# Kernel tuning notes

Measured on AMD Instinct MI355X. Metric: run time of the kernel, lower is better.

## Reference

```python
import jax, jax.numpy as jnp
import numpy as np

B, T, D = 2048, 240, 90  # batch, seq_len (hard-coded 240 in module), hidden
NCLS = 40


def setup_inputs() -> dict:
    key = jax.random.key(0)
    ks = jax.random.split(key, 7)
    s = 1.0 / np.sqrt(D)          # torch LSTMCell init bound
    so = 1.0 / np.sqrt(T * D)     # torch Linear init bound
    x = jax.random.normal(ks[0], (B, T, D), dtype=jnp.float32)
    W_ih = jax.random.uniform(ks[1], (4 * D, D), minval=-s, maxval=s, dtype=jnp.float32)
    W_hh = jax.random.uniform(ks[2], (4 * D, D), minval=-s, maxval=s, dtype=jnp.float32)
    b_ih = jax.random.uniform(ks[3], (4 * D,), minval=-s, maxval=s, dtype=jnp.float32)
    b_hh = jax.random.uniform(ks[4], (4 * D,), minval=-s, maxval=s, dtype=jnp.float32)
    W_out = jax.random.uniform(ks[5], (NCLS, T * D), minval=-so, maxval=so, dtype=jnp.float32)
    b_out = jax.random.uniform(ks[6], (NCLS,), minval=-so, maxval=so, dtype=jnp.float32)
    return {"x": x, "W_ih": W_ih, "W_hh": W_hh, "b_ih": b_ih, "b_hh": b_hh,
            "W_out": W_out, "b_out": b_out}


def reference(x, W_ih, W_hh, b_ih, b_hh, W_out, b_out):
    # The torch loop calls LSTMCell(x[:, i]) with DEFAULT zero (h0, c0) every
    # step -> no recurrence. W_hh @ h0 == 0 and f * c0 == 0, so:
    #   gates = x_t @ W_ih^T + b_ih + b_hh ; gate order i, f, g, o
    gates = jnp.einsum('btd,gd->btg', x, W_ih) + b_ih + b_hh  # [B, T, 4D]
    i_g, _f_g, g_g, o_g = jnp.split(gates, 4, axis=-1)
    c = jax.nn.sigmoid(i_g) * jnp.tanh(g_g)                   # i * g (f*c0 = 0)
    h = jax.nn.sigmoid(o_g) * jnp.tanh(c)                     # [B, T, D]
    out = h.reshape(-1, T * D) @ W_out.T + b_out              # [B, 40]
    out = out.reshape(-1, 4, 10)
    return jax.nn.softmax(out, axis=2)
```

## Files before the change

### kernel.cpp

```cpp
#include <hip/hip_runtime.h>
#include <hip/hip_bf16.h>

#define BB   2048
#define TT   240
#define DD   90
#define MM   (BB*TT)
#define KDIM (TT*DD)
#define NCLS 40
#define NPAD 48
#define KS2  45
#define KST  15

typedef __bf16 bf16x8 __attribute__((ext_vector_type(8)));
typedef float  f32x4  __attribute__((ext_vector_type(4)));

#define LOG2E  1.44269504f
#define LOG2E2 2.88539008f

__device__ __forceinline__ bf16x8 cvt8(float4 a, float4 b){
    bf16x8 r;
    r[0]=(__bf16)a.x; r[1]=(__bf16)a.y; r[2]=(__bf16)a.z; r[3]=(__bf16)a.w;
    r[4]=(__bf16)b.x; r[5]=(__bf16)b.y; r[6]=(__bf16)b.z; r[7]=(__bf16)b.w;
    return r;
}

__device__ __forceinline__ unsigned pack_bf16(float a, float b){
    unsigned u0 = (unsigned)__builtin_bit_cast(unsigned short, (__bf16)a);
    unsigned u1 = (unsigned)__builtin_bit_cast(unsigned short, (__bf16)b);
    return u0 | (u1 << 16);
}

__device__ __forceinline__ float sig_tanh(float a, float b){
    float ea = exp2f(-LOG2E*a);
    float Eb = exp2f(LOG2E2*b);
    return (Eb - 1.f) * __builtin_amdgcn_rcpf((1.f + ea)*(Eb + 1.f));
}

__global__ void pack1(const float* __restrict__ Wih,
                      const float* __restrict__ bih,
                      const float* __restrict__ bhh,
                      __bf16* __restrict__ wtb)
{
    int id = blockIdx.x*256 + threadIdx.x;
    if (id >= 288*13) return;
    int c  = id / 13;
    int k8 = id - c*13;
    int g  = c / 96, dd = c - g*96;
    int row = (g==0 ? dd : (g==1 ? 180+dd : 270+dd));
    float bv = 0.f, bhi = 0.f, blo = 0.f;
    if (dd < 90){
        bv  = bih[row] + bhh[row];
        bhi = (float)(__bf16)bv;
        blo = bv - bhi;
    }
    bf16x8 v;
    #pragma unroll
    for (int e = 0; e < 8; ++e){
        int k = k8*8 + e;
        float f = 0.f;
        if (dd < 90){
            if (k < 90)       f = Wih[row*90 + k];
            else if (k == 90) f = bhi;
            else if (k == 91) f = blo;
        }
        v[e] = (__bf16)f;
    }
    *(bf16x8*)(wtb + c*104 + k8*8) = v;
}

__global__ void pack2(const float* __restrict__ W2,
                      __bf16* __restrict__ w2hi,
                      __bf16* __restrict__ w2lo)
{
    int id = blockIdx.x*256 + threadIdx.x;
    if (id >= NPAD*2700) return;
    int n  = id / 2700;
    int k8 = id - n*2700;
    bf16x8 vh, vl;
    if (n < NCLS){
        #pragma unroll
        for (int e = 0; e < 8; ++e){
            float f = W2[(size_t)n*KDIM + k8*8 + e];
            __bf16 hb = (__bf16)f;
            vh[e] = hb;
            vl[e] = (__bf16)(f - (float)hb);
        }
    } else {
        #pragma unroll
        for (int e = 0; e < 8; ++e){ vh[e] = (__bf16)0.f; vl[e] = (__bf16)0.f; }
    }
    *(bf16x8*)(w2hi + (size_t)n*KDIM + k8*8) = vh;
    *(bf16x8*)(w2lo + (size_t)n*KDIM + k8*8) = vl;
}

__global__ __launch_bounds__(512, 2)
void k1_gates(const float* __restrict__ x,
              const __bf16* __restrict__ wtb,
              __bf16* __restrict__ h)
{
    __shared__ __align__(16) __bf16 wt[288*104];

    const int tid  = threadIdx.x;
    const int lane = tid & 63;
    const int wv   = tid >> 6;
    const int rg   = wv >> 1;
    const int nh   = wv & 1;
    const int l15  = lane & 15;
    const int kg   = lane >> 4;

    {
        const float4* src = (const float4*)wtb;
        float4* dst = (float4*)wt;
        #pragma unroll
        for (int i = 0; i < 8; ++i){
            int idx = tid + i*512;
            if (idx < 3744) dst[idx] = src[idx];
        }
    }
    __syncthreads();

    const int tbase = blockIdx.x * 15;

    float4 xr[6];
    float2 xe;
    {
        const float* p = x + ((size_t)tbase*64 + rg*16 + l15)*90;
        #pragma unroll
        for (int ks = 0; ks < 2; ++ks){
            xr[ks*2+0] = *(const float4*)(p + ks*32 + kg*8);
            xr[ks*2+1] = *(const float4*)(p + ks*32 + kg*8 + 4);
        }
        if (kg < 3){
            xr[4] = *(const float4*)(p + 64 + kg*8);
            xr[5] = *(const float4*)(p + 64 + kg*8 + 4);
        } else {
            xe = *(const float2*)(p + 88);
        }
    }

    for (int t = 0; t < 15; ++t){
        bf16x8 af[3];
        af[0] = cvt8(xr[0], xr[1]);
        af[1] = cvt8(xr[2], xr[3]);
        if (kg < 3){
            af[2] = cvt8(xr[4], xr[5]);
        } else {
            bf16x8 z;
            #pragma unroll
            for (int e = 0; e < 8; ++e) z[e] = (__bf16)0.f;
            z[0] = (__bf16)xe.x; z[1] = (__bf16)xe.y;
            z[2] = (__bf16)1.0f; z[3] = (__bf16)1.0f;
            af[2] = z;
        }

        f32x4 acc[3][3];
        #pragma unroll
        for (int g = 0; g < 3; ++g)
            #pragma unroll
            for (int j = 0; j < 3; ++j) acc[g][j] = f32x4{0.f,0.f,0.f,0.f};

        const __bf16* wbase = wt + (nh*48 + l15)*104 + 8*kg;
        #pragma unroll
        for (int g = 0; g < 3; ++g){
            #pragma unroll
            for (int j = 0; j < 3; ++j){
                const __bf16* wrow = wbase + (g*96 + j*16)*104;
                #pragma unroll
                for (int ks = 0; ks < 3; ++ks){
                    bf16x8 wv8 = *(const bf16x8*)(wrow + ks*32);
                    acc[g][j] = __builtin_amdgcn_mfma_f32_16x16x32_bf16(wv8, af[ks], acc[g][j], 0,0,0);
                }
            }
        }

        if (t < 14){
            const float* p = x + ((size_t)(tbase+t+1)*64 + rg*16 + l15)*90;
            #pragma unroll
            for (int ks = 0; ks < 2; ++ks){
                xr[ks*2+0] = *(const float4*)(p + ks*32 + kg*8);
                xr[ks*2+1] = *(const float4*)(p + ks*32 + kg*8 + 4);
            }
            if (kg < 3){
                xr[4] = *(const float4*)(p + 64 + kg*8);
                xr[5] = *(const float4*)(p + 64 + kg*8 + 4);
            } else {
                xe = *(const float2*)(p + 88);
            }
        }

        const size_t mrow = (size_t)(tbase+t)*64 + rg*16 + l15;
        __bf16* hp = h + mrow*90;
        #pragma unroll
        for (int j = 0; j < 3; ++j){
            int dd0 = nh*48 + j*16 + kg*4;
            float hv[4];
            #pragma unroll
            for (int r = 0; r < 4; ++r){
                float cc = sig_tanh(acc[0][j][r], acc[1][j][r]);
                hv[r]    = sig_tanh(acc[2][j][r], cc);
            }
            if (dd0 < 90)
                *(unsigned*)(hp + dd0) = pack_bf16(hv[0], hv[1]);
            if (dd0 + 2 < 90)
                *(unsigned*)(hp + dd0 + 2) = pack_bf16(hv[2], hv[3]);
        }
    }
}

__global__ __launch_bounds__(256)
void k2_out(const __bf16* __restrict__ h,
            const __bf16* __restrict__ w2hi,
            const __bf16* __restrict__ w2lo,
            float* __restrict__ part2)
{
    const int tid  = threadIdx.x;
    const int lane = tid & 63;
    const int wv   = tid >> 6;
    const int l15  = lane & 15;
    const int kg   = lane >> 4;
    const int m0   = (blockIdx.x*4 + wv) * 32;
    const int chunk= blockIdx.y;
    const size_t kbase = (size_t)chunk*(KST*32) + 8*kg;

    const __bf16* ha = h    + (size_t)(m0 + l15)*KDIM + kbase;
    const __bf16* hb = ha   + (size_t)16*KDIM;
    const __bf16* h0 = w2hi + (size_t)l15*KDIM + kbase;
    const __bf16* h1 = h0   + (size_t)16*KDIM;
    const __bf16* h2 = h0   + (size_t)32*KDIM;
    const __bf16* l0 = w2lo + (size_t)l15*KDIM + kbase;
    const __bf16* l1 = l0   + (size_t)16*KDIM;
    const __bf16* l2 = l0   + (size_t)32*KDIM;

    f32x4 acc00 = {0.f,0.f,0.f,0.f}, acc01 = acc00, acc02 = acc00;
    f32x4 acc10 = acc00, acc11 = acc00, acc12 = acc00;

    #pragma unroll
    for (int s = 0; s < KST; ++s){
        bf16x8 a0  = *(const bf16x8*)(ha + s*32);
        bf16x8 a1  = *(const bf16x8*)(hb + s*32);
        bf16x8 bh0 = *(const bf16x8*)(h0 + s*32);
        bf16x8 bh1 = *(const bf16x8*)(h1 + s*32);
        bf16x8 bh2 = *(const bf16x8*)(h2 + s*32);
        bf16x8 bl0 = *(const bf16x8*)(l0 + s*32);
        bf16x8 bl1 = *(const bf16x8*)(l1 + s*32);
        bf16x8 bl2 = *(const bf16x8*)(l2 + s*32);
        acc00 = __builtin_amdgcn_mfma_f32_16x16x32_bf16(a0, bh0, acc00, 0,0,0);
        acc01 = __builtin_amdgcn_mfma_f32_16x16x32_bf16(a0, bh1, acc01, 0,0,0);
        acc02 = __builtin_amdgcn_mfma_f32_16x16x32_bf16(a0, bh2, acc02, 0,0,0);
        acc10 = __builtin_amdgcn_mfma_f32_16x16x32_bf16(a1, bh0, acc10, 0,0,0);
        acc11 = __builtin_amdgcn_mfma_f32_16x16x32_bf16(a1, bh1, acc11, 0,0,0);
        acc12 = __builtin_amdgcn_mfma_f32_16x16x32_bf16(a1, bh2, acc12, 0,0,0);
        acc00 = __builtin_amdgcn_mfma_f32_16x16x32_bf16(a0, bl0, acc00, 0,0,0);
        acc01 = __builtin_amdgcn_mfma_f32_16x16x32_bf16(a0, bl1, acc01, 0,0,0);
        acc02 = __builtin_amdgcn_mfma_f32_16x16x32_bf16(a0, bl2, acc02, 0,0,0);
        acc10 = __builtin_amdgcn_mfma_f32_16x16x32_bf16(a1, bl0, acc10, 0,0,0);
        acc11 = __builtin_amdgcn_mfma_f32_16x16x32_bf16(a1, bl1, acc11, 0,0,0);
        acc12 = __builtin_amdgcn_mfma_f32_16x16x32_bf16(a1, bl2, acc12, 0,0,0);
    }

    float* pp = part2 + (size_t)chunk*(BB*NPAD);
    const int rbase = kg*4;
    #pragma unroll
    for (int r = 0; r < 4; ++r){
        size_t row0 = (size_t)(m0 + rbase + r)*NPAD;
        size_t row1 = (size_t)(m0 + 16 + rbase + r)*NPAD;
        pp[row0 +      l15] = acc00[r];
        pp[row0 + 16 + l15] = acc01[r];
        pp[row0 + 32 + l15] = acc02[r];
        pp[row1 +      l15] = acc10[r];
        pp[row1 + 16 + l15] = acc11[r];
        pp[row1 + 32 + l15] = acc12[r];
    }
}

__global__ void k3a(const float* __restrict__ part2,
                    const float* __restrict__ bout,
                    float* __restrict__ logits)
{
    int g = blockIdx.x*256 + threadIdx.x;
    float s = 0.f;
    for (int c = 0; c < KS2; ++c) s += part2[(size_t)c*(BB*NPAD) + g];
    int n = g % NPAD;
    logits[g] = s + (n < NCLS ? bout[n] : 0.f);
}

__global__ void k3b(const float* __restrict__ logits, float* __restrict__ out)
{
    int b = blockIdx.x*256 + threadIdx.x;
    if (b >= BB) return;
    const float* lg = logits + (size_t)b*NPAD;
    #pragma unroll
    for (int g = 0; g < 4; ++g){
        float v[10]; float mx = -1e30f;
        #pragma unroll
        for (int q = 0; q < 10; ++q){ v[q] = lg[g*10+q]; mx = fmaxf(mx, v[q]); }
        float e[10]; float s = 0.f;
        #pragma unroll
        for (int q = 0; q < 10; ++q){ e[q] = __expf(v[q]-mx); s += e[q]; }
        float inv = 1.0f/s;
        #pragma unroll
        for (int q = 0; q < 10; ++q) out[(size_t)b*NCLS + g*10 + q] = e[q]*inv;
    }
}

extern "C" void kernel_launch(void* const* d_in, const int* in_sizes, int n_in,
                              void* d_out, int out_size, void* d_ws, size_t ws_size,
                              hipStream_t stream)
{
    const float* x    = (const float*)d_in[0];
    const float* Wih  = (const float*)d_in[1];
    const float* bih  = (const float*)d_in[3];
    const float* bhh  = (const float*)d_in[4];
    const float* W2   = (const float*)d_in[5];
    const float* bout = (const float*)d_in[6];
    float* out = (float*)d_out;

    char* ws = (char*)d_ws;
    size_t off = 0;
    auto alloc = [&](size_t bytes){ void* p = ws + off; off = (off + bytes + 255) & ~(size_t)255; return p; };
    __bf16* h     = (__bf16*)alloc((size_t)MM*DD*2);
    float*  part2 = (float*) alloc((size_t)KS2*BB*NPAD*4);
    float*  logits= (float*) alloc((size_t)BB*NPAD*4);
    __bf16* wtb   = (__bf16*)alloc(288*104*2);
    __bf16* w2hi  = (__bf16*)alloc((size_t)NPAD*KDIM*2);
    __bf16* w2lo  = (__bf16*)alloc((size_t)NPAD*KDIM*2);

    pack1<<<15, 256, 0, stream>>>(Wih, bih, bhh, wtb);
    pack2<<<(NPAD*2700 + 255)/256, 256, 0, stream>>>(W2, w2hi, w2lo);
    k1_gates<<<512, 512, 0, stream>>>(x, wtb, h);
    k2_out<<<dim3(16, KS2), 256, 0, stream>>>(h, w2hi, w2lo, part2);
    k3a<<<(BB*NPAD)/256, 256, 0, stream>>>(part2, bout, logits);
    k3b<<<(BB + 255)/256, 256, 0, stream>>>(logits, out);
}
```

Measured before the change: 138.4 us.

## Pad hidden rows to 96, reorder x prefetch before MFMA, fuse reduction and softmax

The h intermediate is stored with a row stride of 96 instead of 90, so k1 writes full aligned 8-byte chunks without bounds checks, and W_out is repacked with zero-padded columns to match. k2 now covers 16 k-steps per chunk over the padded K. The next x load is issued before the MFMA block so global latency overlaps compute. The split-K reduction and the softmax are fused into one kernel using shared memory, which drops the logits buffer and one launch. The cost is about 7% more bytes for h and for the W_out copies, plus extra MFMA work on the padded zeros.

```diff
diff --git a/kernel.cpp b/kernel.cpp
--- a/kernel.cpp
+++ b/kernel.cpp
@@ -4,12 +4,14 @@
 #define BB   2048
 #define TT   240
 #define DD   90
+#define HD   96
 #define MM   (BB*TT)
 #define KDIM (TT*DD)
+#define KD2  (TT*HD)
 #define NCLS 40
 #define NPAD 48
 #define KS2  45
-#define KST  15
+#define KST  16
 
 typedef __bf16 bf16x8 __attribute__((ext_vector_type(8)));
 typedef float  f32x4  __attribute__((ext_vector_type(4)));
@@ -73,24 +75,22 @@
                       __bf16* __restrict__ w2lo)
 {
     int id = blockIdx.x*256 + threadIdx.x;
-    if (id >= NPAD*2700) return;
-    int n  = id / 2700;
-    int k8 = id - n*2700;
+    if (id >= NPAD*(KD2/8)) return;
+    int n  = id / (KD2/8);
+    int k8 = id - n*(KD2/8);
+    int t  = k8 / 12;
+    int d0 = (k8 - t*12) * 8;
     bf16x8 vh, vl;
-    if (n < NCLS){
-        #pragma unroll
-        for (int e = 0; e < 8; ++e){
-            float f = W2[(size_t)n*KDIM + k8*8 + e];
-            __bf16 hb = (__bf16)f;
-            vh[e] = hb;
-            vl[e] = (__bf16)(f - (float)hb);
-        }
-    } else {
-        #pragma unroll
-        for (int e = 0; e < 8; ++e){ vh[e] = (__bf16)0.f; vl[e] = (__bf16)0.f; }
-    }
-    *(bf16x8*)(w2hi + (size_t)n*KDIM + k8*8) = vh;
-    *(bf16x8*)(w2lo + (size_t)n*KDIM + k8*8) = vl;
+    #pragma unroll
+    for (int e = 0; e < 8; ++e){
+        int d = d0 + e;
+        float f = (n < NCLS && d < 90) ? W2[(size_t)n*KDIM + t*90 + d] : 0.f;
+        __bf16 hb = (__bf16)f;
+        vh[e] = hb;
+        vl[e] = (__bf16)(f - (float)hb);
+    }
+    *(bf16x8*)(w2hi + (size_t)n*KD2 + k8*8) = vh;
+    *(bf16x8*)(w2lo + (size_t)n*KD2 + k8*8) = vl;
 }
 
 __global__ __launch_bounds__(512, 2)
@@ -151,26 +151,6 @@
             z[0] = (__bf16)xe.x; z[1] = (__bf16)xe.y;
             z[2] = (__bf16)1.0f; z[3] = (__bf16)1.0f;
             af[2] = z;
-        }
-
-        f32x4 acc[3][3];
-        #pragma unroll
-        for (int g = 0; g < 3; ++g)
-            #pragma unroll
-            for (int j = 0; j < 3; ++j) acc[g][j] = f32x4{0.f,0.f,0.f,0.f};
-
-        const __bf16* wbase = wt + (nh*48 + l15)*104 + 8*kg;
-        #pragma unroll
-        for (int g = 0; g < 3; ++g){
-            #pragma unroll
-            for (int j = 0; j < 3; ++j){
-                const __bf16* wrow = wbase + (g*96 + j*16)*104;
-                #pragma unroll
-                for (int ks = 0; ks < 3; ++ks){
-                    bf16x8 wv8 = *(const bf16x8*)(wrow + ks*32);
-                    acc[g][j] = __builtin_amdgcn_mfma_f32_16x16x32_bf16(wv8, af[ks], acc[g][j], 0,0,0);
-                }
-            }
         }
 
         if (t < 14){
@@ -188,8 +168,28 @@
             }
         }
 
+        f32x4 acc[3][3];
+        #pragma unroll
+        for (int g = 0; g < 3; ++g)
+            #pragma unroll
+            for (int j = 0; j < 3; ++j) acc[g][j] = f32x4{0.f,0.f,0.f,0.f};
+
+        const __bf16* wbase = wt + (nh*48 + l15)*104 + 8*kg;
+        #pragma unroll
+        for (int g = 0; g < 3; ++g){
+            #pragma unroll
+            for (int j = 0; j < 3; ++j){
+                const __bf16* wrow = wbase + (g*96 + j*16)*104;
+                #pragma unroll
+                for (int ks = 0; ks < 3; ++ks){
+                    bf16x8 wv8 = *(const bf16x8*)(wrow + ks*32);
+                    acc[g][j] = __builtin_amdgcn_mfma_f32_16x16x32_bf16(wv8, af[ks], acc[g][j], 0,0,0);
+                }
+            }
+        }
+
         const size_t mrow = (size_t)(tbase+t)*64 + rg*16 + l15;
-        __bf16* hp = h + mrow*90;
+        __bf16* hp = h + mrow*HD;
         #pragma unroll
         for (int j = 0; j < 3; ++j){
             int dd0 = nh*48 + j*16 + kg*4;
@@ -199,10 +199,10 @@
                 float cc = sig_tanh(acc[0][j][r], acc[1][j][r]);
                 hv[r]    = sig_tanh(acc[2][j][r], cc);
             }
-            if (dd0 < 90)
-                *(unsigned*)(hp + dd0) = pack_bf16(hv[0], hv[1]);
-            if (dd0 + 2 < 90)
-                *(unsigned*)(hp + dd0 + 2) = pack_bf16(hv[2], hv[3]);
+            uint2 pk;
+            pk.x = pack_bf16(hv[0], hv[1]);
+            pk.y = pack_bf16(hv[2], hv[3]);
+            *(uint2*)(hp + dd0) = pk;
         }
     }
 }
@@ -222,14 +222,14 @@
     const int chunk= blockIdx.y;
     const size_t kbase = (size_t)chunk*(KST*32) + 8*kg;
 
-    const __bf16* ha = h    + (size_t)(m0 + l15)*KDIM + kbase;
-    const __bf16* hb = ha   + (size_t)16*KDIM;
-    const __bf16* h0 = w2hi + (size_t)l15*KDIM + kbase;
-    const __bf16* h1 = h0   + (size_t)16*KDIM;
-    const __bf16* h2 = h0   + (size_t)32*KDIM;
-    const __bf16* l0 = w2lo + (size_t)l15*KDIM + kbase;
-    const __bf16* l1 = l0   + (size_t)16*KDIM;
-    const __bf16* l2 = l0   + (size_t)32*KDIM;
+    const __bf16* ha = h    + (size_t)(m0 + l15)*KD2 + kbase;
+    const __bf16* hb = ha   + (size_t)16*KD2;
+    const __bf16* h0 = w2hi + (size_t)l15*KD2 + kbase;
+    const __bf16* h1 = h0   + (size_t)16*KD2;
+    const __bf16* h2 = h0   + (size_t)32*KD2;
+    const __bf16* l0 = w2lo + (size_t)l15*KD2 + kbase;
+    const __bf16* l1 = l0   + (size_t)16*KD2;
+    const __bf16* l2 = l0   + (size_t)32*KD2;
 
     f32x4 acc00 = {0.f,0.f,0.f,0.f}, acc01 = acc00, acc02 = acc00;
     f32x4 acc10 = acc00, acc11 = acc00, acc12 = acc00;
@@ -273,33 +273,38 @@
     }
 }
 
-__global__ void k3a(const float* __restrict__ part2,
-                    const float* __restrict__ bout,
-                    float* __restrict__ logits)
-{
-    int g = blockIdx.x*256 + threadIdx.x;
-    float s = 0.f;
-    for (int c = 0; c < KS2; ++c) s += part2[(size_t)c*(BB*NPAD) + g];
-    int n = g % NPAD;
-    logits[g] = s + (n < NCLS ? bout[n] : 0.f);
-}
-
-__global__ void k3b(const float* __restrict__ logits, float* __restrict__ out)
-{
-    int b = blockIdx.x*256 + threadIdx.x;
-    if (b >= BB) return;
-    const float* lg = logits + (size_t)b*NPAD;
-    #pragma unroll
-    for (int g = 0; g < 4; ++g){
+__global__ __launch_bounds__(384)
+void k3(const float* __restrict__ part2,
+        const float* __restrict__ bout,
+        float* __restrict__ out)
+{
+    __shared__ float sm[8*NPAD];
+    const int tid  = threadIdx.x;
+    const int base = blockIdx.x * 8 * NPAD;
+
+    {
+        int g = base + tid;
+        float s = 0.f;
+        for (int c = 0; c < KS2; ++c) s += part2[(size_t)c*(BB*NPAD) + g];
+        int n = tid % NPAD;
+        sm[tid] = s + (n < NCLS ? bout[n] : 0.f);
+    }
+    __syncthreads();
+
+    if (tid < 32){
+        int lb  = tid >> 2;
+        int grp = tid & 3;
+        const float* lg = sm + lb*NPAD + grp*10;
         float v[10]; float mx = -1e30f;
         #pragma unroll
-        for (int q = 0; q < 10; ++q){ v[q] = lg[g*10+q]; mx = fmaxf(mx, v[q]); }
+        for (int q = 0; q < 10; ++q){ v[q] = lg[q]; mx = fmaxf(mx, v[q]); }
         float e[10]; float s = 0.f;
         #pragma unroll
         for (int q = 0; q < 10; ++q){ e[q] = __expf(v[q]-mx); s += e[q]; }
         float inv = 1.0f/s;
-        #pragma unroll
-        for (int q = 0; q < 10; ++q) out[(size_t)b*NCLS + g*10 + q] = e[q]*inv;
+        size_t b = (size_t)blockIdx.x*8 + lb;
+        #pragma unroll
+        for (int q = 0; q < 10; ++q) out[b*NCLS + grp*10 + q] = e[q]*inv;
     }
 }
 
@@ -318,17 +323,15 @@
     char* ws = (char*)d_ws;
     size_t off = 0;
     auto alloc = [&](size_t bytes){ void* p = ws + off; off = (off + bytes + 255) & ~(size_t)255; return p; };
-    __bf16* h     = (__bf16*)alloc((size_t)MM*DD*2);
+    __bf16* h     = (__bf16*)alloc((size_t)MM*HD*2);
     float*  part2 = (float*) alloc((size_t)KS2*BB*NPAD*4);
-    float*  logits= (float*) alloc((size_t)BB*NPAD*4);
     __bf16* wtb   = (__bf16*)alloc(288*104*2);
-    __bf16* w2hi  = (__bf16*)alloc((size_t)NPAD*KDIM*2);
-    __bf16* w2lo  = (__bf16*)alloc((size_t)NPAD*KDIM*2);
+    __bf16* w2hi  = (__bf16*)alloc((size_t)NPAD*KD2*2);
+    __bf16* w2lo  = (__bf16*)alloc((size_t)NPAD*KD2*2);
 
     pack1<<<15, 256, 0, stream>>>(Wih, bih, bhh, wtb);
-    pack2<<<(NPAD*2700 + 255)/256, 256, 0, stream>>>(W2, w2hi, w2lo);
+    pack2<<<(NPAD*(KD2/8) + 255)/256, 256, 0, stream>>>(W2, w2hi, w2lo);
     k1_gates<<<512, 512, 0, stream>>>(x, wtb, h);
     k2_out<<<dim3(16, KS2), 256, 0, stream>>>(h, w2hi, w2lo, part2);
-    k3a<<<(BB*NPAD)/256, 256, 0, stream>>>(part2, bout, logits);
-    k3b<<<(BB + 255)/256, 256, 0, stream>>>(logits, out);
-}
+    k3<<<BB/8, 384, 0, stream>>>(part2, bout, out);
+}
```

Result: slower. 146.4 us (+5.8%).

## Shrink gate-weight LDS stride, fold exp scales into weights, fuse reduce+softmax

Applied to the files above, without the earlier changes.

The packed W_ih tile in shared memory goes from a 104-element row stride to a dense 92-element stride, which shrinks LDS per block so more k1_gates blocks can share a CU (launch bounds raised to 6). The sigmoid/tanh exp2 scale factors are folded into the packed weights and bias, which removes multiplies from the activation epilogue. The split-K reduction and the softmax are fused into one kernel that stages logits in shared memory, dropping a launch and the logits round trip through global memory. Risks: the 92-element stride is not a multiple of 8, so the 16-byte LDS vector loads may lose alignment or hit bank conflicts. Folding the scale into bf16 weights also changes the rounding.

```diff
diff --git a/kernel.cpp b/kernel.cpp
--- a/kernel.cpp
+++ b/kernel.cpp
@@ -10,6 +10,8 @@
 #define NPAD 48
 #define KS2  45
 #define KST  15
+#define WSTRIDE 92
+#define WELEMS  26512
 
 typedef __bf16 bf16x8 __attribute__((ext_vector_type(8)));
 typedef float  f32x4  __attribute__((ext_vector_type(4)));
@@ -30,42 +32,37 @@
     return u0 | (u1 << 16);
 }
 
-__device__ __forceinline__ float sig_tanh(float a, float b){
-    float ea = exp2f(-LOG2E*a);
-    float Eb = exp2f(LOG2E2*b);
-    return (Eb - 1.f) * __builtin_amdgcn_rcpf((1.f + ea)*(Eb + 1.f));
-}
-
 __global__ void pack1(const float* __restrict__ Wih,
                       const float* __restrict__ bih,
                       const float* __restrict__ bhh,
                       __bf16* __restrict__ wtb)
 {
     int id = blockIdx.x*256 + threadIdx.x;
-    if (id >= 288*13) return;
-    int c  = id / 13;
-    int k8 = id - c*13;
-    int g  = c / 96, dd = c - g*96;
-    int row = (g==0 ? dd : (g==1 ? 180+dd : 270+dd));
-    float bv = 0.f, bhi = 0.f, blo = 0.f;
-    if (dd < 90){
-        bv  = bih[row] + bhh[row];
-        bhi = (float)(__bf16)bv;
-        blo = bv - bhi;
-    }
+    if (id >= WELEMS/8) return;
     bf16x8 v;
     #pragma unroll
     for (int e = 0; e < 8; ++e){
-        int k = k8*8 + e;
+        int el = id*8 + e;
+        int c  = el / WSTRIDE;
+        int k  = el - c*WSTRIDE;
         float f = 0.f;
-        if (dd < 90){
-            if (k < 90)       f = Wih[row*90 + k];
-            else if (k == 90) f = bhi;
-            else if (k == 91) f = blo;
+        if (c < 288){
+            int g = c / 96, dd = c - g*96;
+            if (dd < 90){
+                int row = (g==0 ? dd : (g==1 ? 180+dd : 270+dd));
+                float scale = (g==1) ? LOG2E2 : -LOG2E;
+                if (k < 90){
+                    f = scale * Wih[row*90 + k];
+                } else {
+                    float bv  = scale * (bih[row] + bhh[row]);
+                    float bhi = (float)(__bf16)bv;
+                    f = (k == 90) ? bhi : (bv - bhi);
+                }
+            }
         }
         v[e] = (__bf16)f;
     }
-    *(bf16x8*)(wtb + c*104 + k8*8) = v;
+    *(bf16x8*)(wtb + id*8) = v;
 }
 
 __global__ void pack2(const float* __restrict__ W2,
@@ -93,12 +90,12 @@
     *(bf16x8*)(w2lo + (size_t)n*KDIM + k8*8) = vl;
 }
 
-__global__ __launch_bounds__(512, 2)
+__global__ __launch_bounds__(512, 6)
 void k1_gates(const float* __restrict__ x,
               const __bf16* __restrict__ wtb,
               __bf16* __restrict__ h)
 {
-    __shared__ __align__(16) __bf16 wt[288*104];
+    __shared__ __align__(16) __bf16 wt[WELEMS];
 
     const int tid  = threadIdx.x;
     const int lane = tid & 63;
@@ -112,9 +109,9 @@
         const float4* src = (const float4*)wtb;
         float4* dst = (float4*)wt;
         #pragma unroll
-        for (int i = 0; i < 8; ++i){
+        for (int i = 0; i < 7; ++i){
             int idx = tid + i*512;
-            if (idx < 3744) dst[idx] = src[idx];
+            if (idx < WELEMS/8) dst[idx] = src[idx];
         }
     }
     __syncthreads();
@@ -159,12 +156,12 @@
             #pragma unroll
             for (int j = 0; j < 3; ++j) acc[g][j] = f32x4{0.f,0.f,0.f,0.f};
 
-        const __bf16* wbase = wt + (nh*48 + l15)*104 + 8*kg;
+        const __bf16* wbase = wt + (nh*48 + l15)*WSTRIDE + 8*kg;
         #pragma unroll
         for (int g = 0; g < 3; ++g){
             #pragma unroll
             for (int j = 0; j < 3; ++j){
-                const __bf16* wrow = wbase + (g*96 + j*16)*104;
+                const __bf16* wrow = wbase + (g*96 + j*16)*WSTRIDE;
                 #pragma unroll
                 for (int ks = 0; ks < 3; ++ks){
                     bf16x8 wv8 = *(const bf16x8*)(wrow + ks*32);
@@ -196,8 +193,12 @@
             float hv[4];
             #pragma unroll
             for (int r = 0; r < 4; ++r){
-                float cc = sig_tanh(acc[0][j][r], acc[1][j][r]);
-                hv[r]    = sig_tanh(acc[2][j][r], cc);
+                float ea = exp2f(acc[0][j][r]);
+                float Eg = exp2f(acc[1][j][r]);
+                float cc = (Eg - 1.f) * __builtin_amdgcn_rcpf((1.f + ea)*(Eg + 1.f));
+                float eo = exp2f(acc[2][j][r]);
+                float Ec = exp2f(LOG2E2*cc);
+                hv[r] = (Ec - 1.f) * __builtin_amdgcn_rcpf((1.f + eo)*(Ec + 1.f));
             }
             if (dd0 < 90)
                 *(unsigned*)(hp + dd0) = pack_bf16(hv[0], hv[1]);
@@ -273,33 +274,38 @@
     }
 }
 
-__global__ void k3a(const float* __restrict__ part2,
-                    const float* __restrict__ bout,
-                    float* __restrict__ logits)
-{
-    int g = blockIdx.x*256 + threadIdx.x;
-    float s = 0.f;
-    for (int c = 0; c < KS2; ++c) s += part2[(size_t)c*(BB*NPAD) + g];
-    int n = g % NPAD;
-    logits[g] = s + (n < NCLS ? bout[n] : 0.f);
-}
-
-__global__ void k3b(const float* __restrict__ logits, float* __restrict__ out)
-{
-    int b = blockIdx.x*256 + threadIdx.x;
-    if (b >= BB) return;
-    const float* lg = logits + (size_t)b*NPAD;
-    #pragma unroll
-    for (int g = 0; g < 4; ++g){
+__global__ __launch_bounds__(384)
+void k3(const float* __restrict__ part2,
+        const float* __restrict__ bout,
+        float* __restrict__ out)
+{
+    __shared__ float sm[8*NPAD];
+    const int tid  = threadIdx.x;
+    const int base = blockIdx.x * 8 * NPAD;
+
+    {
+        int g = base + tid;
+        float s = 0.f;
+        for (int c = 0; c < KS2; ++c) s += part2[(size_t)c*(BB*NPAD) + g];
+        int n = tid % NPAD;
+        sm[tid] = s + (n < NCLS ? bout[n] : 0.f);
+    }
+    __syncthreads();
+
+    if (tid < 32){
+        int lb  = tid >> 2;
+        int grp = tid & 3;
+        const float* lg = sm + lb*NPAD + grp*10;
         float v[10]; float mx = -1e30f;
         #pragma unroll
-        for (int q = 0; q < 10; ++q){ v[q] = lg[g*10+q]; mx = fmaxf(mx, v[q]); }
+        for (int q = 0; q < 10; ++q){ v[q] = lg[q]; mx = fmaxf(mx, v[q]); }
         float e[10]; float s = 0.f;
         #pragma unroll
         for (int q = 0; q < 10; ++q){ e[q] = __expf(v[q]-mx); s += e[q]; }
         float inv = 1.0f/s;
-        #pragma unroll
-        for (int q = 0; q < 10; ++q) out[(size_t)b*NCLS + g*10 + q] = e[q]*inv;
+        size_t b = (size_t)blockIdx.x*8 + lb;
+        #pragma unroll
+        for (int q = 0; q < 10; ++q) out[b*NCLS + grp*10 + q] = e[q]*inv;
     }
 }
 
@@ -320,15 +326,13 @@
     auto alloc = [&](size_t bytes){ void* p = ws + off; off = (off + bytes + 255) & ~(size_t)255; return p; };
     __bf16* h     = (__bf16*)alloc((size_t)MM*DD*2);
     float*  part2 = (float*) alloc((size_t)KS2*BB*NPAD*4);
-    float*  logits= (float*) alloc((size_t)BB*NPAD*4);
-    __bf16* wtb   = (__bf16*)alloc(288*104*2);
+    __bf16* wtb   = (__bf16*)alloc((size_t)WELEMS*2);
     __bf16* w2hi  = (__bf16*)alloc((size_t)NPAD*KDIM*2);
     __bf16* w2lo  = (__bf16*)alloc((size_t)NPAD*KDIM*2);
 
-    pack1<<<15, 256, 0, stream>>>(Wih, bih, bhh, wtb);
+    pack1<<<(WELEMS/8 + 255)/256, 256, 0, stream>>>(Wih, bih, bhh, wtb);
     pack2<<<(NPAD*2700 + 255)/256, 256, 0, stream>>>(W2, w2hi, w2lo);
     k1_gates<<<512, 512, 0, stream>>>(x, wtb, h);
     k2_out<<<dim3(16, KS2), 256, 0, stream>>>(h, w2hi, w2lo, part2);
-    k3a<<<(BB*NPAD)/256, 256, 0, stream>>>(part2, bout, logits);
-    k3b<<<(BB + 255)/256, 256, 0, stream>>>(logits, out);
-}
+    k3<<<BB/8, 384, 0, stream>>>(part2, bout, out);
+}
```

Result: slower. 348.4 us (+151.7%).
